# Performance work log

Hardware: AMD Instinct MI355X
Metric: run time of the kernel (lower is better)

## Reference

```python
import jax, jax.numpy as jnp
import numpy as np

N = 50000
E = 1600000
D_IN = 128
D_OUT = 128
K_EIG = 4
N_AGG = 3
N_SCALE = 3
AVG_D_LOG = float(np.log(33.0))  # avg_d['log'] for avg degree 32
BN_EPS = 1e-5


def setup_inputs() -> dict:
    key = jax.random.key(0)
    ks = jax.random.split(key, 8)
    h = jax.random.normal(ks[0], (N, D_IN), dtype=jnp.float32)
    eig = jax.random.normal(ks[1], (N, K_EIG), dtype=jnp.float32)
    snorm_n = jax.random.uniform(ks[2], (N, 1), dtype=jnp.float32)
    edge_src = jax.random.randint(ks[3], (E,), 0, N, dtype=jnp.int32)
    edge_dst = jax.random.randint(ks[4], (E,), 0, N, dtype=jnp.int32)
    d_cat = N_AGG * N_SCALE * D_IN  # 1152
    W = jax.random.normal(ks[5], (d_cat, D_OUT), dtype=jnp.float32) / np.sqrt(d_cat)
    b = jnp.zeros((D_OUT,), dtype=jnp.float32)
    bn_gamma = jnp.ones((D_OUT,), dtype=jnp.float32)
    bn_beta = jnp.zeros((D_OUT,), dtype=jnp.float32)
    bn_mean = jax.random.normal(ks[6], (D_OUT,), dtype=jnp.float32) * 0.1
    bn_var = jnp.ones((D_OUT,), dtype=jnp.float32)
    return {"h": h, "eig": eig, "snorm_n": snorm_n, "W": W, "b": b,
            "bn_gamma": bn_gamma, "bn_beta": bn_beta, "bn_mean": bn_mean,
            "bn_var": bn_var, "edge_src": edge_src, "edge_dst": edge_dst}


def reference(h, eig, snorm_n, W, b, bn_gamma, bn_beta, bn_mean, bn_var, edge_src, edge_dst):
    h_in = h
    # --- pretrans_edges: message e = src h; vector_field = eig_src - eig_dst ---
    h_e = h[edge_src]                      # [E, d] gathered edge messages
    vf = eig[edge_src] - eig[edge_dst]     # [E, k_eig]
    w = jnp.abs(vf[:, 0:1])                # dir1 weights [E, 1]

    # --- reduce: multi-aggregator segment reduce over destination nodes ---
    deg = jax.ops.segment_sum(jnp.ones((E,), h.dtype), edge_dst, num_segments=N)  # [N]
    deg_safe = jnp.maximum(deg, 1.0)
    sum_h = jax.ops.segment_sum(h_e, edge_dst, num_segments=N)
    mean_h = sum_h / deg_safe[:, None]
    max_h = jax.ops.segment_max(h_e, edge_dst, num_segments=N)
    max_h = jnp.where(deg[:, None] > 0, max_h, 0.0)  # empty mailbox -> 0
    dir_num = jax.ops.segment_sum(h_e * w, edge_dst, num_segments=N)
    dir_den = jax.ops.segment_sum(w, edge_dst, num_segments=N)  # [N, 1]
    dir_av = dir_num / (dir_den + 1e-30)
    agg = jnp.concatenate([mean_h, max_h, dir_av], axis=1)  # [N, 3d]

    # --- scalers: identity, amplification, attenuation ---
    logD = jnp.log(deg + 1.0)[:, None]
    amp = agg * (logD / AVG_D_LOG)
    att = agg * (AVG_D_LOG / jnp.maximum(logD, 1e-6))
    hcat = jnp.concatenate([agg, amp, att], axis=1)  # [N, 9d]

    # --- posttrans MLP (1 layer, no activation) ---
    out = hcat @ W + b
    # graph norm
    out = out * snorm_n
    # batch norm (eval mode, running stats)
    out = (out - bn_mean) * jax.lax.rsqrt(bn_var + BN_EPS) * bn_gamma + bn_beta
    out = jax.nn.relu(out)
    # residual (in_dim == out_dim)
    out = h_in + out
    # dropout p=0.0 / eval -> identity
    return out
```

## Files before the change

kernel.cpp:

```cpp
#include <hip/hip_runtime.h>
#include <hip/hip_bf16.h>

#define DIN 128
#define KEIG 4
#define BSH 7
#define BCAP 5120
#define ITEMS 16
#define AVG_D_LOG 3.4965075614664802f
#define BN_EPS 1e-5f

typedef __attribute__((ext_vector_type(8))) short bf16x8;
typedef __attribute__((ext_vector_type(4))) float f32x4;
typedef __attribute__((ext_vector_type(2))) float f32x2;

#define GLD16(SRC, DST) __builtin_amdgcn_global_load_lds(                     \
    (const __attribute__((address_space(1))) unsigned int*)(const void*)(SRC),\
    (__attribute__((address_space(3))) unsigned int*)(void*)(DST), 16, 0, 0)

static __device__ inline unsigned short f2bf(float f) {
    union { float f; unsigned u; } v; v.f = f;
    unsigned r = v.u + 0x7FFFu + ((v.u >> 16) & 1u);
    return (unsigned short)(r >> 16);
}
static __device__ inline unsigned pack2bf(float lo, float hi) {
    return (unsigned)f2bf(lo) | ((unsigned)f2bf(hi) << 16);
}
static __device__ inline f32x2 up2(unsigned u) {
    f32x2 r;
    r.x = __int_as_float(u << 16);
    r.y = __int_as_float(u & 0xffff0000u);
    return r;
}


__global__ void k_pb(const float* __restrict__ h, unsigned* __restrict__ hb,
                     const float* __restrict__ W, unsigned short* __restrict__ Wt,
                     const float* __restrict__ eig,
                     const int* __restrict__ src, const int* __restrict__ dst,
                     int* __restrict__ bcur, uint2* __restrict__ stag,
                     int nPairs, int wTotal, int E, int nbk, int gridB)
{
    __shared__ int lcnt[512];
    __shared__ int lbase[512];
    const int t = threadIdx.x;

    if ((int)blockIdx.x < gridB) {
        for (int b = t; b < nbk; b += 256) lcnt[b] = 0;
        __syncthreads();

        const int e0 = blockIdx.x * (256 * ITEMS);
        int   bky[ITEMS];
        int   rnk[ITEMS];
        uint2 rec[ITEMS];
#pragma unroll
        for (int k = 0; k < ITEMS; ++k) {
            const int e = e0 + t + k * 256;
            if (e < E) {
                const int s = src[e], d = dst[e];
                const float w = fabsf(eig[(size_t)s * KEIG] - eig[(size_t)d * KEIG]);
                rec[k] = make_uint2(((unsigned)f2bf(w) << 16) | (unsigned)s, (unsigned)d);
                bky[k] = d >> BSH;
                rnk[k] = atomicAdd(&lcnt[bky[k]], 1);
            } else bky[k] = -1;
        }
        __syncthreads();
        for (int b = t; b < nbk; b += 256) {
            const int c = lcnt[b];
            lbase[b] = c ? atomicAdd(&bcur[b], c) : 0;
        }
        __syncthreads();
#pragma unroll
        for (int k = 0; k < ITEMS; ++k) {
            if (bky[k] >= 0) {
                const int pos = lbase[bky[k]] + rnk[k];
                if (pos < BCAP) stag[(size_t)bky[k] * BCAP + pos] = rec[k];
            }
        }
    } else {
        const int i = ((int)blockIdx.x - gridB) * 256 + t;
        if (i < nPairs) {
            float2 v = reinterpret_cast<const float2*>(h)[i];
            hb[i] = pack2bf(v.x, v.y);
        }
        if (i < wTotal) {
            int k = i % 384;
            int rest = i / 384;
            int col = rest & 127;
            int s = rest >> 7;
            const int ks = k >> 5, kg = (k >> 3) & 3, ko = k & 7;
            const int c = s * 8 + kg * 2 + (col >> 6);
            const int lane = col & 63;
            const size_t idx = (size_t)ks * 12288 + c * 512 + lane * 8 + ko;
            Wt[idx] = f2bf(W[(s * 384 + k) * 128 + col]);
        }
    }
}


__global__ void k_group(const int* __restrict__ bcur, const uint2* __restrict__ stag,
                        unsigned* __restrict__ final_, int2* __restrict__ offcnt, int N)
{
    __shared__ uint2 sst[BCAP];
    __shared__ int hcnt[128];
    __shared__ int sbuf[2][128];
    const int b = blockIdx.x;
    const int t = threadIdx.x;
    const int cb = min(bcur[b], BCAP);

    for (int i = t; i < cb; i += 256) sst[i] = stag[(size_t)b * BCAP + i];
    if (t < 128) hcnt[t] = 0;
    __syncthreads();

    int dl[(BCAP + 255) / 256];
    int rk[(BCAP + 255) / 256];
    int nit = 0;
    for (int i = t; i < cb; i += 256) {
        const int d_loc = sst[i].y & 127;
        dl[nit] = d_loc;
        rk[nit] = atomicAdd(&hcnt[d_loc], 1);
        ++nit;
    }
    __syncthreads();

    int cur = 0;
    if (t < 128) sbuf[0][t] = hcnt[t];
    __syncthreads();
    for (int d = 1; d < 128; d <<= 1) {
        if (t < 128) {
            int x = sbuf[cur][t];
            if (t >= d) x += sbuf[cur][t - d];
            sbuf[cur ^ 1][t] = x;
        }
        cur ^= 1;
        __syncthreads();
    }
    const int exb = cur ^ 1;
    if (t < 128) sbuf[exb][t] = sbuf[cur][t] - hcnt[t];
    __syncthreads();

    if (t < 128) {
        const int dg = (b << BSH) + t;
        if (dg < N) offcnt[dg] = make_int2(b * BCAP + sbuf[exb][t], hcnt[t]);
    }
    nit = 0;
    for (int i = t; i < cb; i += 256) {
        final_[(size_t)b * BCAP + sbuf[exb][dl[nit]] + rk[nit]] = sst[i].x;
        ++nit;
    }
}


__global__ void k_prep(const float* __restrict__ h, unsigned* __restrict__ hb,
                       const float* __restrict__ W, unsigned short* __restrict__ Wt,
                       const float* __restrict__ eig, float* __restrict__ eig0,
                       int* __restrict__ cursor, int* __restrict__ bcur,
                       int nPairs, int wTotal, int N, int nbk)
{
    int i = blockIdx.x * 256 + threadIdx.x;
    if (i < nPairs) {
        float2 v = reinterpret_cast<const float2*>(h)[i];
        hb[i] = pack2bf(v.x, v.y);
    }
    if (i < wTotal) {
        int k = i % 384;
        int rest = i / 384;
        int col = rest & 127;
        int s = rest >> 7;
        const int ks = k >> 5, kg = (k >> 3) & 3, ko = k & 7;
        const int c = s * 8 + kg * 2 + (col >> 6);
        const int lane = col & 63;
        const size_t idx = (size_t)ks * 12288 + c * 512 + lane * 8 + ko;
        Wt[idx] = f2bf(W[(s * 384 + k) * 128 + col]);
    }
    if (i < N) {
        eig0[i] = eig[(size_t)i * KEIG];
        cursor[i] = 0;
    }
    if (i < nbk) bcur[i] = 0;
}

__global__ void k_hist(const int* __restrict__ dst, int* __restrict__ counts, int E) {
    int e = blockIdx.x * 256 + threadIdx.x;
    if (e < E) atomicAdd(&counts[dst[e]], 1);
}

__global__ void k_part(const int* __restrict__ counts, int* __restrict__ part, int N) {
    __shared__ int red[4];
    const int t = threadIdx.x;
    const int i = blockIdx.x * 256 + t;
    int v = (i < N) ? counts[i] : 0;
    for (int d = 32; d >= 1; d >>= 1) v += __shfl_down(v, d, 64);
    if ((t & 63) == 0) red[t >> 6] = v;
    __syncthreads();
    if (t == 0) part[blockIdx.x] = red[0] + red[1] + red[2] + red[3];
}

__global__ void k_scan1(const int* __restrict__ part, int* __restrict__ partoff,
                        int* __restrict__ total_out, int NB) {
    __shared__ int buf[2][256];
    const int t = threadIdx.x;
    int v = (t < NB) ? part[t] : 0;
    buf[0][t] = v;
    __syncthreads();
    int cur = 0;
    for (int d = 1; d < 256; d <<= 1) {
        int x = buf[cur][t];
        if (t >= d) x += buf[cur][t - d];
        buf[cur ^ 1][t] = x;
        cur ^= 1;
        __syncthreads();
    }
    if (t < NB) partoff[t] = buf[cur][t] - v;
    if (t == 255) *total_out = buf[cur][255];
}

__global__ void k_off(const int* __restrict__ counts, const int* __restrict__ partoff,
                      int* __restrict__ offsets, int* __restrict__ cursor, int N) {
    __shared__ int buf[2][256];
    const int t = threadIdx.x;
    const int i = blockIdx.x * 256 + t;
    int v = (i < N) ? counts[i] : 0;
    buf[0][t] = v;
    __syncthreads();
    int cur = 0;
    for (int d = 1; d < 256; d <<= 1) {
        int x = buf[cur][t];
        if (t >= d) x += buf[cur][t - d];
        buf[cur ^ 1][t] = x;
        cur ^= 1;
        __syncthreads();
    }
    if (i < N) {
        int excl = partoff[blockIdx.x] + buf[cur][t] - v;
        offsets[i] = excl;
        cursor[i]  = excl;
    }
}

__global__ void k_fill_csr(const int* __restrict__ src, const int* __restrict__ dst,
                           const float* __restrict__ eig0, int* __restrict__ cursor,
                           int2* __restrict__ sedge, int E)
{
    int e = blockIdx.x * 256 + threadIdx.x;
    if (e < E) {
        int s = src[e], d = dst[e];
        float w = fabsf(eig0[s] - eig0[d]);
        int pos = atomicAdd(&cursor[d], 1);
        sedge[pos] = make_int2(s, __float_as_int(w));
    }
}


template<bool PACKED>
__launch_bounds__(256, 4)
__global__ void k_agg(const unsigned* __restrict__ hb,
                      const int2* __restrict__ offcnt, const int* __restrict__ offsets,
                      const unsigned* __restrict__ upk, const int2* __restrict__ sedge,
                      unsigned short* __restrict__ agg, float2* __restrict__ scal, int N)
{
    const int tid = threadIdx.x;
    const int qid = tid >> 4;
    const int l16 = tid & 15;
    const int n = blockIdx.x * 16 + qid;
    if (n >= N) return;

    int e0, cnt;
    if (PACKED) { const int2 oc = offcnt[n]; e0 = oc.x; cnt = oc.y; }
    else        { e0 = offsets[n]; cnt = offsets[n + 1] - e0; }

    const uint4* __restrict__ hb4 = reinterpret_cast<const uint4*>(hb);

    f32x2 s2[4], m2[4], d2[4];
    float wsum = 0.f;
#pragma unroll
    for (int f = 0; f < 4; ++f) {
        s2[f] = (f32x2){0.f, 0.f};
        m2[f] = (f32x2){-INFINITY, -INFINITY};
        d2[f] = (f32x2){0.f, 0.f};
    }
    const int clampi = (cnt > 0) ? cnt - 1 : 0;

    uint4 bufA[8], bufB[8];
    float wvA[8], wvB[8];

#define STAGE(BUF, WV, BASE) do {                                        \
    _Pragma("unroll")                                                    \
    for (int j = 0; j < 8; ++j) {                                        \
        int ci = (BASE) + j; ci = ci < clampi ? ci : clampi;             \
        unsigned sidx;                                                   \
        if (PACKED) {                                                    \
            const unsigned u = upk[e0 + ci];                             \
            WV[j] = __int_as_float(u & 0xffff0000u);                     \
            sidx = (u & 0xffffu) << 4;                                   \
        } else {                                                         \
            const int2 v = sedge[e0 + ci];                               \
            WV[j] = __int_as_float(v.y);                                 \
            sidx = ((unsigned)v.x) << 4;                                 \
        }                                                                \
        BUF[j] = hb4[sidx | (unsigned)l16];                              \
    }                                                                    \
} while (0)

#define ACCUM(BUF, WV, BASE) do {                                        \
    _Pragma("unroll")                                                    \
    for (int j = 0; j < 8; ++j) {                                        \
        if ((BASE) + j < cnt) {                                          \
            const float wj = WV[j];                                      \
            const f32x2 wj2 = (f32x2){wj, wj};                           \
            const f32x2 p0 = up2(BUF[j].x), p1 = up2(BUF[j].y);          \
            const f32x2 p2 = up2(BUF[j].z), p3 = up2(BUF[j].w);          \
            s2[0] += p0; s2[1] += p1; s2[2] += p2; s2[3] += p3;          \
            m2[0].x = fmaxf(m2[0].x, p0.x); m2[0].y = fmaxf(m2[0].y, p0.y); \
            m2[1].x = fmaxf(m2[1].x, p1.x); m2[1].y = fmaxf(m2[1].y, p1.y); \
            m2[2].x = fmaxf(m2[2].x, p2.x); m2[2].y = fmaxf(m2[2].y, p2.y); \
            m2[3].x = fmaxf(m2[3].x, p3.x); m2[3].y = fmaxf(m2[3].y, p3.y); \
            d2[0] += p0 * wj2; d2[1] += p1 * wj2;                        \
            d2[2] += p2 * wj2; d2[3] += p3 * wj2;                        \
            wsum += wj;                                                  \
        }                                                                \
    }                                                                    \
} while (0)

    if (cnt > 0) {
        STAGE(bufA, wvA, 0);
        for (int base = 0; base < cnt; base += 16) {
            const bool haveB = (base + 8) < cnt;
            if (haveB) STAGE(bufB, wvB, base + 8);
            ACCUM(bufA, wvA, base);
            if (base + 16 < cnt) STAGE(bufA, wvA, base + 16);
            if (haveB) ACCUM(bufB, wvB, base + 8);
        }
    }
#undef STAGE
#undef ACCUM

    const float degf = (float)cnt;
    const float inv  = 1.0f / fmaxf(degf, 1.0f);
    const float dinv = 1.0f / (wsum + 1e-30f);
    const bool nz = (cnt > 0);
    uint4 pm, px, pd;
    pm.x = pack2bf(s2[0].x * inv, s2[0].y * inv);
    pm.y = pack2bf(s2[1].x * inv, s2[1].y * inv);
    pm.z = pack2bf(s2[2].x * inv, s2[2].y * inv);
    pm.w = pack2bf(s2[3].x * inv, s2[3].y * inv);
    px.x = pack2bf(nz ? m2[0].x : 0.f, nz ? m2[0].y : 0.f);
    px.y = pack2bf(nz ? m2[1].x : 0.f, nz ? m2[1].y : 0.f);
    px.z = pack2bf(nz ? m2[2].x : 0.f, nz ? m2[2].y : 0.f);
    px.w = pack2bf(nz ? m2[3].x : 0.f, nz ? m2[3].y : 0.f);
    pd.x = pack2bf(d2[0].x * dinv, d2[0].y * dinv);
    pd.y = pack2bf(d2[1].x * dinv, d2[1].y * dinv);
    pd.z = pack2bf(d2[2].x * dinv, d2[2].y * dinv);
    pd.w = pack2bf(d2[3].x * dinv, d2[3].y * dinv);

    uint4* aggv = reinterpret_cast<uint4*>(agg);
    const int mt = n >> 6, row = n & 63;
    const size_t b4 = (size_t)mt * 3072 + (size_t)(l16 & 3) * 64 + row;
    const int kshi = l16 >> 2;
    aggv[b4 + (size_t)(0 * 4 + kshi) * 256] = pm;
    aggv[b4 + (size_t)(1 * 4 + kshi) * 256] = px;
    aggv[b4 + (size_t)(2 * 4 + kshi) * 256] = pd;
    if (l16 == 0) {
        const float logD = logf(degf + 1.0f);
        scal[n] = make_float2(logD / AVG_D_LOG, AVG_D_LOG / fmaxf(logD, 1e-6f));
    }
}


__launch_bounds__(256, 2)
__global__ void k_mm(const unsigned short* __restrict__ agg, const float2* __restrict__ scal,
                     const float* __restrict__ h, const float* __restrict__ snorm,
                     const float* __restrict__ bvec, const float* __restrict__ gam,
                     const float* __restrict__ bet, const float* __restrict__ bmean,
                     const float* __restrict__ bvar, const unsigned short* __restrict__ Wt,
                     float* __restrict__ out, int N, int nT)
{
    __shared__ char smem[65536];
    char* AsB = smem;
    char* BsB = smem + 16384;
    float* outS = (float*)smem;

    const int tid  = threadIdx.x;
    const int wave = tid >> 6;
    const int lane = tid & 63;
    const int r16  = lane & 15;
    const int kgrp = lane >> 4;
    const int cb = wave * 32;

    const int mt0 = blockIdx.x * 2;
    const int mt1 = (mt0 + 1 < nT) ? (mt0 + 1) : mt0;
    const char* aggb0 = (const char*)agg + (size_t)mt0 * 49152;
    const char* aggb1 = (const char*)agg + (size_t)mt1 * 49152;
    const char* wtbase = (const char*)Wt;

    auto stage = [&](int ks, int bf) {
        GLD16(aggb0 + (size_t)ks * 4096 + wave * 1024 + lane * 16,
              AsB + (size_t)bf * 8192 + wave * 1024);
        GLD16(aggb1 + (size_t)ks * 4096 + wave * 1024 + lane * 16,
              AsB + (size_t)bf * 8192 + 4096 + wave * 1024);
#pragma unroll
        for (int i = 0; i < 6; ++i) {
            const int c = wave * 6 + i;
            GLD16(wtbase + (size_t)ks * 24576 + (size_t)c * 1024 + lane * 16,
                  BsB + (size_t)bf * 24576 + (size_t)c * 1024);
        }
    };

    f32x4 acc[2][4][2][3];
#pragma unroll
    for (int t = 0; t < 2; ++t)
#pragma unroll
        for (int m = 0; m < 4; ++m)
#pragma unroll
            for (int ct = 0; ct < 2; ++ct)
#pragma unroll
                for (int sv = 0; sv < 3; ++sv)
                    acc[t][m][ct][sv] = (f32x4){0.f, 0.f, 0.f, 0.f};

    stage(0, 0);
    for (int ks = 0; ks < 12; ++ks) {
        const int bf = ks & 1;
        __syncthreads();
        if (ks + 1 < 12) stage(ks + 1, bf ^ 1);

        bf16x8 a0[4], a1[4], b[6];
#pragma unroll
        for (int m = 0; m < 4; ++m) {
            a0[m] = *reinterpret_cast<const bf16x8*>(
                AsB + (size_t)bf * 8192 + ((size_t)kgrp * 64 + m * 16 + r16) * 16);
            a1[m] = *reinterpret_cast<const bf16x8*>(
                AsB + (size_t)bf * 8192 + 4096 + ((size_t)kgrp * 64 + m * 16 + r16) * 16);
        }
#pragma unroll
        for (int sv = 0; sv < 3; ++sv)
#pragma unroll
            for (int ct = 0; ct < 2; ++ct)
                b[sv * 2 + ct] = *reinterpret_cast<const bf16x8*>(
                    BsB + (size_t)bf * 24576 +
                    (((size_t)sv * 4 + kgrp) * 128 + cb + ct * 16 + r16) * 16);
#pragma unroll
        for (int sv = 0; sv < 3; ++sv)
#pragma unroll
            for (int ct = 0; ct < 2; ++ct)
#pragma unroll
                for (int m = 0; m < 4; ++m) {
                    acc[0][m][ct][sv] = __builtin_amdgcn_mfma_f32_16x16x32_bf16(
                        a0[m], b[sv * 2 + ct], acc[0][m][ct][sv], 0, 0, 0);
                    acc[1][m][ct][sv] = __builtin_amdgcn_mfma_f32_16x16x32_bf16(
                        a1[m], b[sv * 2 + ct], acc[1][m][ct][sv], 0, 0, 0);
                }
    }

    __syncthreads();
#pragma unroll
    for (int t = 0; t < 2; ++t) {
        if (t == 1 && mt1 == mt0) break;
        const int nb = (t ? mt1 : mt0) * 64;
#pragma unroll
        for (int ct = 0; ct < 2; ++ct) {
            const int col = cb + ct * 16 + r16;
            const float bc  = bvec[col];
            const float mc  = bmean[col];
            const float rs  = rsqrtf(bvar[col] + BN_EPS);
            const float gc  = gam[col];
            const float bec = bet[col];
#pragma unroll
            for (int m = 0; m < 4; ++m) {
#pragma unroll
                for (int r = 0; r < 4; ++r) {
                    const int row = m * 16 + kgrp * 4 + r;
                    const int n  = nb + row;
                    float sn = 0.f; float2 sc = make_float2(0.f, 0.f);
                    if (n < N) { sn = snorm[n]; sc = scal[n]; }
                    float v = acc[t][m][ct][0][r] + sc.x * acc[t][m][ct][1][r]
                                                  + sc.y * acc[t][m][ct][2][r];
                    float y = (v + bc) * sn;
                    y = (y - mc) * rs * gc + bec;
                    y = fmaxf(y, 0.f);
                    outS[row * 132 + col] = y;
                }
            }
        }
        __syncthreads();
        const int rows = (N - nb < 64) ? (N - nb) : 64;
#pragma unroll
        for (int it = 0; it < 8; ++it) {
            const int idx = it * 256 + tid;
            const int row = idx >> 5;
            const int c4  = idx & 31;
            if (row < rows) {
                const float4 hv = *reinterpret_cast<const float4*>(
                    &h[(size_t)(nb + row) * 128 + c4 * 4]);
                float4 yv = *reinterpret_cast<const float4*>(&outS[row * 132 + c4 * 4]);
                yv.x += hv.x; yv.y += hv.y; yv.z += hv.z; yv.w += hv.w;
                *reinterpret_cast<float4*>(&out[(size_t)(nb + row) * 128 + c4 * 4]) = yv;
            }
        }
        __syncthreads();
    }
}


extern "C" void kernel_launch(void* const* d_in, const int* in_sizes, int n_in,
                              void* d_out, int out_size, void* d_ws, size_t ws_size,
                              hipStream_t stream)
{
    const float* h     = (const float*)d_in[0];
    const float* eig   = (const float*)d_in[1];
    const float* snorm = (const float*)d_in[2];
    const float* W     = (const float*)d_in[3];
    const float* bvec  = (const float*)d_in[4];
    const float* gam   = (const float*)d_in[5];
    const float* bet   = (const float*)d_in[6];
    const float* bmean = (const float*)d_in[7];
    const float* bvar  = (const float*)d_in[8];
    const int*   esrc  = (const int*)d_in[9];
    const int*   edst  = (const int*)d_in[10];
    float* out = (float*)d_out;

    const int N = in_sizes[0] / DIN;
    const int E = in_sizes[9];
    const int NB = (N + 255) / 256;
    const int nPairs = N * DIN / 2;
    const int wTotal = 3 * 128 * 384;
    const int nbk = (N + 127) >> BSH;
    const int N64 = (N + 63) / 64;
    const int N128 = (N + 127) / 128;
    (void)ws_size; (void)n_in; (void)out_size;

    char* base = (char*)d_ws;
    size_t o = 0;
    auto take = [&](size_t bytes) {
        char* p = base + o;
        o = (o + bytes + 255) & ~(size_t)255;
        return p;
    };
    unsigned* hb       = (unsigned*)take((size_t)nPairs * 4);
    unsigned short* Wt = (unsigned short*)take((size_t)wTotal * 2);
    float* eig0        = (float*)take((size_t)N * 4);
    int* cursor        = (int*)take((size_t)(N + 1) * 4);
    float2* scal       = (float2*)take((size_t)N * 8);

    const size_t agg_bytes  = (size_t)N64 * 49152;
    const size_t stag_bytes = (size_t)nbk * BCAP * 8;
    const size_t shared_bytes = agg_bytes > stag_bytes ? agg_bytes : stag_bytes;

    const size_t bucket_bytes = (size_t)nbk * BCAP * 4
                              + (size_t)N * 8
                              + (size_t)nbk * 4
                              + shared_bytes + 8192;
    const bool bucketOK = (N <= 65536) && (nbk <= 512) && ((o + bucket_bytes) <= ws_size);

    const int gridPrep = (nPairs + 255) / 256;
    const int gridE    = (E + 255) / 256;
    const int gridB    = (E + 256 * ITEMS - 1) / (256 * ITEMS);
    const int gridN16  = (N + 15) / 16;

    if (bucketOK) {
        unsigned* fin   = (unsigned*)take((size_t)nbk * BCAP * 4);
        int2* offcnt    = (int2*)take((size_t)N * 8);
        int* bcur       = (int*)take((size_t)nbk * 4);
        char* shared    = take(shared_bytes);
        uint2* stag     = (uint2*)shared;
        unsigned short* agg = (unsigned short*)shared;

        hipMemsetAsync(bcur, 0, (size_t)nbk * 4, stream);
        k_pb<<<gridB + gridPrep, 256, 0, stream>>>(h, hb, W, Wt, eig, esrc, edst,
                                                   bcur, stag, nPairs, wTotal, E,
                                                   nbk, gridB);
        k_group<<<nbk, 256, 0, stream>>>(bcur, stag, fin, offcnt, N);
        k_agg<true><<<gridN16, 256, 0, stream>>>(hb, offcnt, nullptr, fin, nullptr,
                                                 agg, scal, N);
        k_mm<<<N128, 256, 0, stream>>>(agg, scal, h, snorm, bvec, gam, bet, bmean, bvar,
                                       Wt, out, N, N64);
    } else {
        int* counts  = (int*)take((size_t)(N + 1) * 4);
        int* offsets = (int*)take((size_t)(N + 1) * 4);
        int2* sedge  = (int2*)take((size_t)(E + 16) * 8);
        int* part    = (int*)take((size_t)NB * 4);
        int* partoff = (int*)take((size_t)NB * 4);
        int* bcur    = (int*)take(4096);
        unsigned short* agg = (unsigned short*)take(agg_bytes);

        k_prep<<<gridPrep, 256, 0, stream>>>(h, hb, W, Wt, eig, eig0, counts, bcur,
                                             nPairs, wTotal, N, 1);
        k_hist<<<gridE, 256, 0, stream>>>(edst, counts, E);
        k_part<<<NB, 256, 0, stream>>>(counts, part, N);
        k_scan1<<<1, 256, 0, stream>>>(part, partoff, &offsets[N], NB);
        k_off<<<NB, 256, 0, stream>>>(counts, partoff, offsets, cursor, N);
        k_fill_csr<<<gridE, 256, 0, stream>>>(esrc, edst, eig0, cursor, sedge, E);
        k_agg<false><<<gridN16, 256, 0, stream>>>(hb, nullptr, offsets, nullptr, sedge,
                                                  agg, scal, N);
        k_mm<<<N128, 256, 0, stream>>>(agg, scal, h, snorm, bvec, gam, bet, bmean, bvar,
                                       Wt, out, N, N64);
    }
}
```

Before: 153.0 us.

## Single-buffer GEMM LDS staging and use packed max in aggregation

The matmul kernel drops its double-buffered LDS staging. It now loads each K-slice into a single buffer, synchronises, computes, then synchronises again, which cuts shared memory from 64KB to about 33KB so more blocks can be resident per CU. The price is that global-to-LDS loads no longer overlap with MFMA work, so each step exposes load latency. Separately, the segment-max accumulation uses a packed vector max builtin instead of scalar fmaxf pairs, aiming for packed max instructions.

```diff
diff --git a/kernel.cpp b/kernel.cpp
--- a/kernel.cpp
+++ b/kernel.cpp
@@ -30,6 +30,13 @@
     r.x = __int_as_float(u << 16);
     r.y = __int_as_float(u & 0xffff0000u);
     return r;
+}
+static __device__ inline f32x2 pkmax(f32x2 a, f32x2 b) {
+#if __has_builtin(__builtin_elementwise_max)
+    return __builtin_elementwise_max(a, b);
+#else
+    a.x = fmaxf(a.x, b.x); a.y = fmaxf(a.y, b.y); return a;
+#endif
 }
 
 
@@ -310,10 +317,8 @@
             const f32x2 p0 = up2(BUF[j].x), p1 = up2(BUF[j].y);          \
             const f32x2 p2 = up2(BUF[j].z), p3 = up2(BUF[j].w);          \
             s2[0] += p0; s2[1] += p1; s2[2] += p2; s2[3] += p3;          \
-            m2[0].x = fmaxf(m2[0].x, p0.x); m2[0].y = fmaxf(m2[0].y, p0.y); \
-            m2[1].x = fmaxf(m2[1].x, p1.x); m2[1].y = fmaxf(m2[1].y, p1.y); \
-            m2[2].x = fmaxf(m2[2].x, p2.x); m2[2].y = fmaxf(m2[2].y, p2.y); \
-            m2[3].x = fmaxf(m2[3].x, p3.x); m2[3].y = fmaxf(m2[3].y, p3.y); \
+            m2[0] = pkmax(m2[0], p0); m2[1] = pkmax(m2[1], p1);          \
+            m2[2] = pkmax(m2[2], p2); m2[3] = pkmax(m2[3], p3);          \
             d2[0] += p0 * wj2; d2[1] += p1 * wj2;                        \
             d2[2] += p2 * wj2; d2[3] += p3 * wj2;                        \
             wsum += wj;                                                  \
@@ -374,9 +379,9 @@
                      const float* __restrict__ bvar, const unsigned short* __restrict__ Wt,
                      float* __restrict__ out, int N, int nT)
 {
-    __shared__ char smem[65536];
-    char* AsB = smem;
-    char* BsB = smem + 16384;
+    __shared__ char smem[33792];
+    unsigned short* As = (unsigned short*)smem;
+    unsigned short* Bs = (unsigned short*)(smem + 8192);
     float* outS = (float*)smem;
 
     const int tid  = threadIdx.x;
@@ -392,16 +397,16 @@
     const char* aggb1 = (const char*)agg + (size_t)mt1 * 49152;
     const char* wtbase = (const char*)Wt;
 
-    auto stage = [&](int ks, int bf) {
+    auto stage = [&](int ks) {
         GLD16(aggb0 + (size_t)ks * 4096 + wave * 1024 + lane * 16,
-              AsB + (size_t)bf * 8192 + wave * 1024);
+              (char*)As + (size_t)wave * 1024);
         GLD16(aggb1 + (size_t)ks * 4096 + wave * 1024 + lane * 16,
-              AsB + (size_t)bf * 8192 + 4096 + wave * 1024);
+              (char*)As + (size_t)(4 + wave) * 1024);
 #pragma unroll
         for (int i = 0; i < 6; ++i) {
             const int c = wave * 6 + i;
             GLD16(wtbase + (size_t)ks * 24576 + (size_t)c * 1024 + lane * 16,
-                  BsB + (size_t)bf * 24576 + (size_t)c * 1024);
+                  (char*)Bs + (size_t)c * 1024);
         }
     };
 
@@ -416,27 +421,25 @@
                 for (int sv = 0; sv < 3; ++sv)
                     acc[t][m][ct][sv] = (f32x4){0.f, 0.f, 0.f, 0.f};
 
-    stage(0, 0);
     for (int ks = 0; ks < 12; ++ks) {
-        const int bf = ks & 1;
-        __syncthreads();
-        if (ks + 1 < 12) stage(ks + 1, bf ^ 1);
+        if (ks) __syncthreads();
+        stage(ks);
+        __syncthreads();
 
         bf16x8 a0[4], a1[4], b[6];
 #pragma unroll
         for (int m = 0; m < 4; ++m) {
             a0[m] = *reinterpret_cast<const bf16x8*>(
-                AsB + (size_t)bf * 8192 + ((size_t)kgrp * 64 + m * 16 + r16) * 16);
+                &As[((size_t)kgrp * 64 + m * 16 + r16) * 8]);
             a1[m] = *reinterpret_cast<const bf16x8*>(
-                AsB + (size_t)bf * 8192 + 4096 + ((size_t)kgrp * 64 + m * 16 + r16) * 16);
+                &As[((size_t)(4 + kgrp) * 64 + m * 16 + r16) * 8]);
         }
 #pragma unroll
         for (int sv = 0; sv < 3; ++sv)
 #pragma unroll
             for (int ct = 0; ct < 2; ++ct)
                 b[sv * 2 + ct] = *reinterpret_cast<const bf16x8*>(
-                    BsB + (size_t)bf * 24576 +
-                    (((size_t)sv * 4 + kgrp) * 128 + cb + ct * 16 + r16) * 16);
+                    &Bs[(((size_t)sv * 4 + kgrp) * 128 + cb + ct * 16 + r16) * 8]);
 #pragma unroll
         for (int sv = 0; sv < 3; ++sv)
 #pragma unroll
```

New measurement: 151.8 us. No clear change (-0.8%).
